# Performance work log

Hardware: AMD Instinct MI355X
Metric: run time of the kernel (lower is better)

## Reference

```python
import jax, jax.numpy as jnp
import numpy as np

N = 100000   # nodes
E = 50000    # hyperedges
K = 4        # nodes per hyperedge
D = 128      # out_dim (= in_dim here)
ED = 64      # edge_dim
H = 8        # num_heads


def _build_pairs(seed=0):
    # Sparse equivalent of the incidence-matrix nested loops:
    # for each edge e with member set S, emit ordered pairs (v, e, u) for v,u in S.
    rng = np.random.default_rng(seed)
    cover = rng.permutation(N).reshape(N // K, K)          # guarantees every node owns >=1 pair group
    rand = rng.integers(0, N, size=(E - N // K, K))
    edge_nodes = np.concatenate([cover, rand], axis=0)      # [E, K]
    owners = np.repeat(edge_nodes, K, axis=1).ravel()       # v, repeated K times per edge slot
    pair_u = np.tile(edge_nodes, (1, K)).ravel()            # u, tiled
    pair_e = np.repeat(np.arange(E), K * K)
    return owners.astype(np.int32), pair_e.astype(np.int32), pair_u.astype(np.int32)


def setup_inputs() -> dict:
    key = jax.random.key(0)
    ks = jax.random.split(key, 12)
    owners, pair_e, pair_u = _build_pairs()
    s = 0.05
    return {
        "x": jax.random.normal(ks[0], (N, D), jnp.float32),
        "edge_attr": jax.random.normal(ks[1], (E, ED), jnp.float32),
        "w_lin": jax.random.normal(ks[2], (D, D), jnp.float32) * s,   # self.lin (no bias)
        "w_e": jax.random.normal(ks[3], (ED, D), jnp.float32) * s,    # self.edge_lin (no bias)
        "w_q": jax.random.normal(ks[4], (D, D), jnp.float32) * s,
        "b_q": jax.random.normal(ks[5], (D,), jnp.float32) * s,
        "w_k": jax.random.normal(ks[6], (D, D), jnp.float32) * s,
        "b_k": jax.random.normal(ks[7], (D,), jnp.float32) * s,
        "w_v": jax.random.normal(ks[8], (D, D), jnp.float32) * s,
        "b_v": jax.random.normal(ks[9], (D,), jnp.float32) * s,
        "w_o": jax.random.normal(ks[10], (D, D), jnp.float32) * s,
        "b_o": jax.random.normal(ks[11], (D,), jnp.float32) * s,
        "owners": jnp.asarray(owners),
        "pair_e": jnp.asarray(pair_e),
        "pair_u": jnp.asarray(pair_u),
    }


def reference(x, edge_attr, w_lin, w_e, w_q, b_q, w_k, b_k, w_v, b_v, w_o, b_o, owners, pair_e, pair_u):
    n = x.shape[0]
    d = w_lin.shape[1]
    dh = d // H
    Wh = x @ w_lin                                  # [N, D]
    We = edge_attr @ w_e                            # [E, D]
    # Multi-head single-query attention per node over its (e,u) pair set.
    q = ((Wh @ w_q + b_q) / jnp.sqrt(jnp.asarray(dh, Wh.dtype))).reshape(n, H, dh)
    Wh_u = Wh[pair_u]                               # [P, D] value source (= Wh[u])
    k = ((Wh_u + We[pair_e]) @ w_k + b_k).reshape(-1, H, dh)   # key source = Wh[u] + We[e]
    v = (Wh_u @ w_v + b_v).reshape(-1, H, dh)
    scores = jnp.einsum('phd,phd->ph', q[owners], k)            # [P, H]
    # segmented (ragged) softmax over each node's pair set
    m = jax.ops.segment_max(scores, owners, num_segments=n)
    ex = jnp.exp(scores - m[owners])
    denom = jax.ops.segment_sum(ex, owners, num_segments=n)     # [N, H]
    alpha = ex / denom[owners]                                  # [P, H]
    ctx = jax.ops.segment_sum(alpha[..., None] * v, owners, num_segments=n).reshape(n, d)
    out = ctx @ w_o + b_o
    return jax.nn.relu(out)
```

## Files before the change

kernel.cpp:

```cpp
#include <hip/hip_runtime.h>

#define NN 100000
#define EE 50000
#define GG (EE*4)
#define NB 391

typedef __attribute__((ext_vector_type(8))) short bf16x8;
typedef __attribute__((ext_vector_type(4))) float f32x4;

__device__ __forceinline__ unsigned short f2bf(float f) {
  union { float f; unsigned int u; } c; c.f = f;
  unsigned int u = c.u;
  u = (u + 0x7fffu + ((u >> 16) & 1u)) >> 16;
  return (unsigned short)u;
}
__device__ __forceinline__ float bf2f(unsigned int lo16) {
  union { unsigned int u; float f; } c; c.u = lo16 << 16;
  return c.f;
}

struct __align__(8) us4 { unsigned short x, y, z, w; };

__global__ void k_prep(const float* __restrict__ w_lin, const float* __restrict__ w_e,
                       const float* __restrict__ w_q, const float* __restrict__ b_q,
                       const float* __restrict__ w_k, const float* __restrict__ b_k,
                       const float* __restrict__ w_v, const float* __restrict__ b_v,
                       const float* __restrict__ w_o, const float* __restrict__ b_o,
                       unsigned short* __restrict__ WT, unsigned short* __restrict__ WeT,
                       unsigned short* __restrict__ WoT, float* __restrict__ bias384,
                       float* __restrict__ bkB, float* __restrict__ boB) {
  int t = blockIdx.x * 256 + threadIdx.x;
  if (t < 49152) {
    int n = t >> 7, k = t & 127;
    const float* wsel; int nn; float scale = 1.0f;
    if (n < 128)      { wsel = w_q; nn = n;       scale = 0.25f; }
    else if (n < 256) { wsel = w_k; nn = n - 128; }
    else              { wsel = w_v; nn = n - 256; }
    float s = 0.f;
    for (int d = 0; d < 128; ++d) s += w_lin[k*128 + d] * wsel[d*128 + nn];
    WT[n*128 + k] = f2bf(s * scale);
  } else if (t < 57344) {
    int i = t - 49152, n = i >> 6, k = i & 63;
    float s = 0.f;
    for (int d = 0; d < 128; ++d) s += w_e[k*128 + d] * w_k[d*128 + n];
    WeT[n*64 + k] = f2bf(s);
  } else if (t < 73728) {
    int i = t - 57344, n = i >> 7, k = i & 127;
    WoT[n*128 + k] = f2bf(w_o[k*128 + n]);
  } else if (t < 74112) {
    int i = t - 73728;
    bias384[i] = (i < 128) ? b_q[i] * 0.25f : ((i < 256) ? 0.f : b_v[i - 256]);
  } else if (t < 74240) {
    bkB[t - 74112] = b_k[t - 74112];
  } else if (t < 74368) {
    boB[t - 74240] = b_o[t - 74240];
  }
}

__global__ __launch_bounds__(256) void k_qkv(const float* __restrict__ x,
                                             const unsigned short* __restrict__ WT,
                                             const float* __restrict__ bias,
                                             unsigned short* __restrict__ qkv) {
  __shared__ unsigned short As[64 * 136];
  int tid = threadIdx.x;
  int row0 = blockIdx.x * 64;
  #pragma unroll
  for (int it = 0; it < 8; ++it) {
    int i4 = tid + it * 256;
    int r = i4 >> 5, c4 = i4 & 31;
    float4 vv = make_float4(0.f, 0.f, 0.f, 0.f);
    int gr = row0 + r;
    if (gr < NN) vv = *(const float4*)(x + (size_t)gr * 128 + c4 * 4);
    us4 s4 = { f2bf(vv.x), f2bf(vv.y), f2bf(vv.z), f2bf(vv.w) };
    int chunk = c4 >> 1;
    int soff = r * 128 + ((chunk ^ (r & 7)) << 3) + ((c4 & 1) << 2);
    *(us4*)(&As[soff]) = s4;
  }
  __syncthreads();
  int w = tid >> 6, lane = tid & 63, lr = lane & 15, lk = lane >> 4;
  bf16x8 afr[4][4];
  #pragma unroll
  for (int rt = 0; rt < 4; ++rt) {
    int R = rt * 16 + lr;
    #pragma unroll
    for (int kk = 0; kk < 4; ++kk) {
      int chunk = (kk * 4 + lk) ^ (R & 7);
      afr[rt][kk] = *(const bf16x8*)(&As[R * 128 + chunk * 8]);
    }
  }
  #pragma unroll
  for (int p = 0; p < 3; ++p) {
    f32x4 acc[2][4] = {};
    #pragma unroll
    for (int h = 0; h < 2; ++h) {
      int gcol = p * 128 + h * 64 + w * 16 + lr;
      const unsigned short* bp = WT + (size_t)gcol * 128 + lk * 8;
      bf16x8 b0 = *(const bf16x8*)(bp);
      bf16x8 b1 = *(const bf16x8*)(bp + 32);
      bf16x8 b2 = *(const bf16x8*)(bp + 64);
      bf16x8 b3 = *(const bf16x8*)(bp + 96);
      #pragma unroll
      for (int rt = 0; rt < 4; ++rt) {
        acc[h][rt] = __builtin_amdgcn_mfma_f32_16x16x32_bf16(afr[rt][0], b0, acc[h][rt], 0, 0, 0);
        acc[h][rt] = __builtin_amdgcn_mfma_f32_16x16x32_bf16(afr[rt][1], b1, acc[h][rt], 0, 0, 0);
        acc[h][rt] = __builtin_amdgcn_mfma_f32_16x16x32_bf16(afr[rt][2], b2, acc[h][rt], 0, 0, 0);
        acc[h][rt] = __builtin_amdgcn_mfma_f32_16x16x32_bf16(afr[rt][3], b3, acc[h][rt], 0, 0, 0);
      }
    }
    __syncthreads();
    #pragma unroll
    for (int h = 0; h < 2; ++h) {
      int colp = h * 64 + w * 16 + lr;
      float b = bias[p * 128 + colp];
      #pragma unroll
      for (int rt = 0; rt < 4; ++rt) {
        #pragma unroll
        for (int j = 0; j < 4; ++j) {
          As[(rt * 16 + lk * 4 + j) * 136 + colp] = f2bf(acc[h][rt][j] + b);
        }
      }
    }
    __syncthreads();
    int piece = tid & 15, rbase = tid >> 4;
    #pragma unroll
    for (int it = 0; it < 4; ++it) {
      int r = rbase + it * 16;
      int grow = row0 + r;
      if (grow < NN) {
        float4 vv = *(const float4*)(&As[r * 136 + piece * 8]);
        *(float4*)(qkv + (size_t)grow * 384 + p * 128 + piece * 8) = vv;
      }
    }
  }
}

__global__ __launch_bounds__(256) void k_ke(const float* __restrict__ ea,
                                            const unsigned short* __restrict__ WeT,
                                            const float* __restrict__ bk,
                                            unsigned short* __restrict__ ke) {
  __shared__ unsigned short As[64][72];
  __shared__ unsigned short Bs[64][72];
  int tid = threadIdx.x;
  int row0 = blockIdx.x * 64;
  int col0 = blockIdx.y * 64;
  #pragma unroll
  for (int it = 0; it < 4; ++it) {
    int i4 = tid + it * 256;
    int r = i4 >> 4, c4 = i4 & 15;
    float4 vv = make_float4(0.f, 0.f, 0.f, 0.f);
    int gr = row0 + r;
    if (gr < EE) vv = *(const float4*)(ea + (size_t)gr * 64 + c4 * 4);
    us4 s4 = { f2bf(vv.x), f2bf(vv.y), f2bf(vv.z), f2bf(vv.w) };
    *(us4*)(&As[r][c4 * 4]) = s4;
  }
  #pragma unroll
  for (int it = 0; it < 4; ++it) {
    int i4 = tid + it * 256;
    int r = i4 >> 4, c4 = i4 & 15;
    us4 s4 = *(const us4*)(WeT + (size_t)(col0 + r) * 64 + c4 * 4);
    *(us4*)(&Bs[r][c4 * 4]) = s4;
  }
  __syncthreads();
  int w = tid >> 6, lane = tid & 63, lr = lane & 15, lk = lane >> 4;
  f32x4 acc[4] = {};
  #pragma unroll
  for (int kk = 0; kk < 2; ++kk) {
    int kof = kk * 32 + lk * 8;
    bf16x8 af = *(const bf16x8*)(&As[w * 16 + lr][kof]);
    #pragma unroll
    for (int nt = 0; nt < 4; ++nt) {
      bf16x8 bfrag = *(const bf16x8*)(&Bs[nt * 16 + lr][kof]);
      acc[nt] = __builtin_amdgcn_mfma_f32_16x16x32_bf16(af, bfrag, acc[nt], 0, 0, 0);
    }
  }
  #pragma unroll
  for (int nt = 0; nt < 4; ++nt) {
    int gcol = col0 + nt * 16 + lr;
    float b = bk[gcol];
    #pragma unroll
    for (int j = 0; j < 4; ++j) {
      int grow = row0 + w * 16 + lk * 4 + j;
      if (grow < EE) ke[(size_t)grow * 128 + gcol] = f2bf(acc[nt][j] + b);
    }
  }
}

__global__ void k_count(const int* __restrict__ owners, int* __restrict__ counts) {
  int g = blockIdx.x * 256 + threadIdx.x;
  if (g < GG) atomicAdd(counts + owners[(size_t)g * 4], 1);
}

__global__ __launch_bounds__(256) void k_scan1(const int* __restrict__ counts,
                                               int* __restrict__ lofs,
                                               int* __restrict__ bsums) {
  __shared__ int tmp[256];
  int tid = threadIdx.x;
  int i = blockIdx.x * 256 + tid;
  int v = (i < NN) ? counts[i] : 0;
  tmp[tid] = v;
  __syncthreads();
  int val = v;
  #pragma unroll
  for (int off = 1; off < 256; off <<= 1) {
    int t = (tid >= off) ? tmp[tid - off] : 0;
    __syncthreads();
    val += t;
    tmp[tid] = val;
    __syncthreads();
  }
  if (i < NN) lofs[i] = val - v;
  if (tid == 255) bsums[blockIdx.x] = val;
}

__global__ __launch_bounds__(512) void k_scan2(int* __restrict__ bsums) {
  __shared__ int tmp[512];
  int tid = threadIdx.x;
  int v = (tid < NB) ? bsums[tid] : 0;
  tmp[tid] = v;
  __syncthreads();
  int val = v;
  #pragma unroll
  for (int off = 1; off < 512; off <<= 1) {
    int t = (tid >= off) ? tmp[tid - off] : 0;
    __syncthreads();
    val += t;
    tmp[tid] = val;
    __syncthreads();
  }
  if (tid < NB) bsums[tid] = val - v;
}

__global__ void k_scan3(const int* __restrict__ lofs, const int* __restrict__ bsums,
                        int* __restrict__ starts, int* __restrict__ wcursor) {
  int i = blockIdx.x * 256 + threadIdx.x;
  if (i < NN) {
    int s = lofs[i] + bsums[i >> 8];
    starts[i] = s;
    wcursor[i] = s;
  }
  if (i == 0) starts[NN] = GG;
}

__global__ void k_scatter(const int* __restrict__ owners, int* __restrict__ wcursor,
                          int* __restrict__ pos) {
  int g = blockIdx.x * 256 + threadIdx.x;
  if (g < GG) {
    int v = owners[(size_t)g * 4];
    pos[g] = atomicAdd(wcursor + v, 1);
  }
}

__global__ __launch_bounds__(256) void k_edge(const unsigned short* __restrict__ qkv,
                                              const unsigned short* __restrict__ ke,
                                              const int* __restrict__ pair_u,
                                              const int* __restrict__ pos,
                                              unsigned short* __restrict__ pctx,
                                              float* __restrict__ pden) {
  int e = blockIdx.x * 4 + (threadIdx.x >> 6);
  if (e >= EE) return;
  int lane = threadIdx.x & 63;
  int m[4], ps[4];
  #pragma unroll
  for (int j = 0; j < 4; ++j) {
    m[j]  = __builtin_amdgcn_readfirstlane(pair_u[(size_t)e * 16 + j]);
    ps[j] = __builtin_amdgcn_readfirstlane(pos[(size_t)e * 4 + j]);
  }
  unsigned int kew = *(const unsigned int*)(ke + (size_t)e * 128 + 2 * lane);
  float e0 = bf2f(kew & 0xffffu), e1 = bf2f(kew >> 16);
  float qa[4][2], ka[4][2], va[4][2];
  #pragma unroll
  for (int j = 0; j < 4; ++j) {
    const unsigned short* r = qkv + (size_t)m[j] * 384 + 2 * lane;
    unsigned int qw = *(const unsigned int*)r;
    unsigned int kw = *(const unsigned int*)(r + 128);
    unsigned int vw = *(const unsigned int*)(r + 256);
    qa[j][0] = bf2f(qw & 0xffffu);      qa[j][1] = bf2f(qw >> 16);
    ka[j][0] = bf2f(kw & 0xffffu) + e0; ka[j][1] = bf2f(kw >> 16) + e1;
    va[j][0] = bf2f(vw & 0xffffu);      va[j][1] = bf2f(vw >> 16);
  }
  #pragma unroll
  for (int i = 0; i < 4; ++i) {
    float c0 = 0.f, c1 = 0.f, ds = 0.f;
    #pragma unroll
    for (int j = 0; j < 4; ++j) {
      float sc = qa[i][0] * ka[j][0] + qa[i][1] * ka[j][1];
      sc += __shfl_xor(sc, 1);
      sc += __shfl_xor(sc, 2);
      sc += __shfl_xor(sc, 4);
      float ex = __expf(sc);
      c0 += ex * va[j][0];
      c1 += ex * va[j][1];
      ds += ex;
    }
    unsigned int packed = (unsigned int)f2bf(c0) | ((unsigned int)f2bf(c1) << 16);
    *(unsigned int*)(pctx + (size_t)ps[i] * 128 + 2 * lane) = packed;
    if ((lane & 7) == 0) pden[(size_t)ps[i] * 8 + (lane >> 3)] = ds;
  }
}

__global__ __launch_bounds__(256) void k_out(const unsigned short* __restrict__ pctx,
                                             const float* __restrict__ pden,
                                             const int* __restrict__ starts,
                                             const unsigned short* __restrict__ WoT,
                                             const float* __restrict__ bo,
                                             float* __restrict__ out) {
  __shared__ unsigned short As[64][136];
  __shared__ unsigned short Bs[128][136];
  int tid = threadIdx.x;
  int row0 = blockIdx.x * 64;
  #pragma unroll
  for (int it = 0; it < 8; ++it) {
    int i4 = tid + it * 256;
    int r = i4 >> 5, c4 = i4 & 31;
    int gr = row0 + r;
    float a0 = 0.f, a1 = 0.f, a2 = 0.f, a3 = 0.f, ds = 0.f;
    if (gr < NN) {
      int s0 = starts[gr], s1 = starts[gr + 1];
      for (int sl = s0; sl < s1; ++sl) {
        us4 wv = *(const us4*)(pctx + (size_t)sl * 128 + c4 * 4);
        a0 += bf2f(wv.x); a1 += bf2f(wv.y); a2 += bf2f(wv.z); a3 += bf2f(wv.w);
        ds += pden[(size_t)sl * 8 + (c4 >> 2)];
      }
    }
    float inv = ds > 0.f ? 1.0f / ds : 0.f;
    us4 s4 = { f2bf(a0 * inv), f2bf(a1 * inv), f2bf(a2 * inv), f2bf(a3 * inv) };
    *(us4*)(&As[r][c4 * 4]) = s4;
  }
  #pragma unroll
  for (int it = 0; it < 16; ++it) {
    int i4 = tid + it * 256;
    int r = i4 >> 5, c4 = i4 & 31;
    *(us4*)(&Bs[r][c4 * 4]) = *(const us4*)(WoT + (size_t)r * 128 + c4 * 4);
  }
  __syncthreads();
  int w = tid >> 6, lane = tid & 63, lr = lane & 15, lk = lane >> 4;
  f32x4 acc[8] = {};
  #pragma unroll
  for (int kk = 0; kk < 4; ++kk) {
    int kof = kk * 32 + lk * 8;
    bf16x8 af = *(const bf16x8*)(&As[w * 16 + lr][kof]);
    #pragma unroll
    for (int nt = 0; nt < 8; ++nt) {
      bf16x8 bfrag = *(const bf16x8*)(&Bs[nt * 16 + lr][kof]);
      acc[nt] = __builtin_amdgcn_mfma_f32_16x16x32_bf16(af, bfrag, acc[nt], 0, 0, 0);
    }
  }
  #pragma unroll
  for (int nt = 0; nt < 8; ++nt) {
    int gcol = nt * 16 + lr;
    float b = bo[gcol];
    #pragma unroll
    for (int j = 0; j < 4; ++j) {
      int grow = row0 + w * 16 + lk * 4 + j;
      if (grow < NN) {
        float vvv = acc[nt][j] + b;
        out[(size_t)grow * 128 + gcol] = vvv > 0.f ? vvv : 0.f;
      }
    }
  }
}

extern "C" void kernel_launch(void* const* d_in, const int* in_sizes, int n_in,
                              void* d_out, int out_size, void* d_ws, size_t ws_size,
                              hipStream_t stream) {
  const float* x      = (const float*)d_in[0];
  const float* ea     = (const float*)d_in[1];
  const float* w_lin  = (const float*)d_in[2];
  const float* w_e    = (const float*)d_in[3];
  const float* w_q    = (const float*)d_in[4];
  const float* b_q    = (const float*)d_in[5];
  const float* w_k    = (const float*)d_in[6];
  const float* b_k    = (const float*)d_in[7];
  const float* w_v    = (const float*)d_in[8];
  const float* b_v    = (const float*)d_in[9];
  const float* w_o    = (const float*)d_in[10];
  const float* b_o    = (const float*)d_in[11];
  const int* owners   = (const int*)d_in[12];
  const int* pair_u   = (const int*)d_in[14];
  float* out = (float*)d_out;

  char* base = (char*)d_ws;
  size_t o = 0;
  auto alloc = [&](size_t b) {
    void* p = base + o;
    o = (o + b + 255) & ~(size_t)255;
    return p;
  };
  unsigned short* WT      = (unsigned short*)alloc((size_t)384 * 128 * 2);
  unsigned short* WeT     = (unsigned short*)alloc((size_t)128 * 64 * 2);
  unsigned short* WoT     = (unsigned short*)alloc((size_t)128 * 128 * 2);
  float* bias384          = (float*)alloc(384 * 4);
  float* bkB              = (float*)alloc(128 * 4);
  float* boB              = (float*)alloc(128 * 4);
  unsigned short* qkv     = (unsigned short*)alloc((size_t)NN * 384 * 2);
  unsigned short* keb     = (unsigned short*)alloc((size_t)EE * 128 * 2);
  int* counts             = (int*)alloc((size_t)NN * 4);
  int* starts             = (int*)alloc((size_t)(NN + 1) * 4);
  int* wcursor            = (int*)alloc((size_t)NN * 4);
  int* pos                = (int*)alloc((size_t)GG * 4);
  int* lofs               = (int*)alloc((size_t)NN * 4);
  int* bsums              = (int*)alloc((size_t)NB * 4);
  unsigned short* pctx    = (unsigned short*)alloc((size_t)GG * 128 * 2);
  float* pden             = (float*)alloc((size_t)GG * 8 * 4);

  hipMemsetAsync(counts, 0, (size_t)NN * 4, stream);

  k_prep<<<291, 256, 0, stream>>>(w_lin, w_e, w_q, b_q, w_k, b_k, w_v, b_v, w_o, b_o,
                                  WT, WeT, WoT, bias384, bkB, boB);
  k_qkv<<<1563, 256, 0, stream>>>(x, WT, bias384, qkv);
  k_ke<<<dim3(782, 2), 256, 0, stream>>>(ea, WeT, bkB, keb);
  k_count<<<782, 256, 0, stream>>>(owners, counts);
  k_scan1<<<NB, 256, 0, stream>>>(counts, lofs, bsums);
  k_scan2<<<1, 512, 0, stream>>>(bsums);
  k_scan3<<<NB, 256, 0, stream>>>(lofs, bsums, starts, wcursor);
  k_scatter<<<782, 256, 0, stream>>>(owners, wcursor, pos);
  k_edge<<<12500, 256, 0, stream>>>(qkv, keb, pair_u, pos, pctx, pden);
  k_out<<<1563, 256, 0, stream>>>(pctx, pden, starts, WoT, boB, out);
}
```

Measured before the change: 180.7 us.

## Drop LDS staging in output GEMM and process two hyperedges per wave

k_out no longer stages aggregated context rows and the Wo matrix in shared memory behind a block barrier. Each wave now gathers and normalizes 16 node rows straight into MFMA B-fragments, reads Wo fragments directly from global memory, and computes a transposed 16x16 product whose result is written as float4 stores. k_edge now handles two hyperedges per wave, raising memory-level parallelism on the gathered qkv rows and halving the grid. The trade-offs are more register pressure in both kernels and repeated global (cache-served) reads of Wo per wave instead of one shared copy per block.

```diff
diff --git a/kernel.cpp b/kernel.cpp
--- a/kernel.cpp
+++ b/kernel.cpp
@@ -17,6 +17,13 @@
 __device__ __forceinline__ float bf2f(unsigned int lo16) {
   union { unsigned int u; float f; } c; c.u = lo16 << 16;
   return c.f;
+}
+__device__ __forceinline__ bf16x8 pack8(const float* f) {
+  union { bf16x8 v; unsigned int u[4]; } r;
+  #pragma unroll
+  for (int i = 0; i < 4; ++i)
+    r.u[i] = (unsigned int)f2bf(f[2*i]) | ((unsigned int)f2bf(f[2*i+1]) << 16);
+  return r.v;
 }
 
 struct __align__(8) us4 { unsigned short x, y, z, w; };
@@ -256,46 +263,56 @@
                                               const int* __restrict__ pos,
                                               unsigned short* __restrict__ pctx,
                                               float* __restrict__ pden) {
-  int e = blockIdx.x * 4 + (threadIdx.x >> 6);
-  if (e >= EE) return;
+  int e0 = (blockIdx.x * 4 + (threadIdx.x >> 6)) * 2;
+  if (e0 >= EE) return;
   int lane = threadIdx.x & 63;
-  int m[4], ps[4];
-  #pragma unroll
-  for (int j = 0; j < 4; ++j) {
-    m[j]  = __builtin_amdgcn_readfirstlane(pair_u[(size_t)e * 16 + j]);
-    ps[j] = __builtin_amdgcn_readfirstlane(pos[(size_t)e * 4 + j]);
-  }
-  unsigned int kew = *(const unsigned int*)(ke + (size_t)e * 128 + 2 * lane);
-  float e0 = bf2f(kew & 0xffffu), e1 = bf2f(kew >> 16);
-  float qa[4][2], ka[4][2], va[4][2];
-  #pragma unroll
-  for (int j = 0; j < 4; ++j) {
-    const unsigned short* r = qkv + (size_t)m[j] * 384 + 2 * lane;
-    unsigned int qw = *(const unsigned int*)r;
-    unsigned int kw = *(const unsigned int*)(r + 128);
-    unsigned int vw = *(const unsigned int*)(r + 256);
-    qa[j][0] = bf2f(qw & 0xffffu);      qa[j][1] = bf2f(qw >> 16);
-    ka[j][0] = bf2f(kw & 0xffffu) + e0; ka[j][1] = bf2f(kw >> 16) + e1;
-    va[j][0] = bf2f(vw & 0xffffu);      va[j][1] = bf2f(vw >> 16);
-  }
-  #pragma unroll
-  for (int i = 0; i < 4; ++i) {
-    float c0 = 0.f, c1 = 0.f, ds = 0.f;
+  int m[2][4], ps[2][4];
+  #pragma unroll
+  for (int ee = 0; ee < 2; ++ee)
     #pragma unroll
     for (int j = 0; j < 4; ++j) {
-      float sc = qa[i][0] * ka[j][0] + qa[i][1] * ka[j][1];
-      sc += __shfl_xor(sc, 1);
-      sc += __shfl_xor(sc, 2);
-      sc += __shfl_xor(sc, 4);
-      float ex = __expf(sc);
-      c0 += ex * va[j][0];
-      c1 += ex * va[j][1];
-      ds += ex;
-    }
-    unsigned int packed = (unsigned int)f2bf(c0) | ((unsigned int)f2bf(c1) << 16);
-    *(unsigned int*)(pctx + (size_t)ps[i] * 128 + 2 * lane) = packed;
-    if ((lane & 7) == 0) pden[(size_t)ps[i] * 8 + (lane >> 3)] = ds;
-  }
+      m[ee][j]  = __builtin_amdgcn_readfirstlane(pair_u[(size_t)(e0 + ee) * 16 + j]);
+      ps[ee][j] = __builtin_amdgcn_readfirstlane(pos[(size_t)(e0 + ee) * 4 + j]);
+    }
+  float ev[2][2];
+  #pragma unroll
+  for (int ee = 0; ee < 2; ++ee) {
+    unsigned int kew = *(const unsigned int*)(ke + (size_t)(e0 + ee) * 128 + 2 * lane);
+    ev[ee][0] = bf2f(kew & 0xffffu); ev[ee][1] = bf2f(kew >> 16);
+  }
+  float qa[2][4][2], ka[2][4][2], va[2][4][2];
+  #pragma unroll
+  for (int ee = 0; ee < 2; ++ee)
+    #pragma unroll
+    for (int j = 0; j < 4; ++j) {
+      const unsigned short* r = qkv + (size_t)m[ee][j] * 384 + 2 * lane;
+      unsigned int qw = *(const unsigned int*)r;
+      unsigned int kw = *(const unsigned int*)(r + 128);
+      unsigned int vw = *(const unsigned int*)(r + 256);
+      qa[ee][j][0] = bf2f(qw & 0xffffu);             qa[ee][j][1] = bf2f(qw >> 16);
+      ka[ee][j][0] = bf2f(kw & 0xffffu) + ev[ee][0]; ka[ee][j][1] = bf2f(kw >> 16) + ev[ee][1];
+      va[ee][j][0] = bf2f(vw & 0xffffu);             va[ee][j][1] = bf2f(vw >> 16);
+    }
+  #pragma unroll
+  for (int ee = 0; ee < 2; ++ee)
+    #pragma unroll
+    for (int i = 0; i < 4; ++i) {
+      float c0 = 0.f, c1 = 0.f, ds = 0.f;
+      #pragma unroll
+      for (int j = 0; j < 4; ++j) {
+        float sc = qa[ee][i][0] * ka[ee][j][0] + qa[ee][i][1] * ka[ee][j][1];
+        sc += __shfl_xor(sc, 1);
+        sc += __shfl_xor(sc, 2);
+        sc += __shfl_xor(sc, 4);
+        float ex = __expf(sc);
+        c0 += ex * va[ee][j][0];
+        c1 += ex * va[ee][j][1];
+        ds += ex;
+      }
+      unsigned int packed = (unsigned int)f2bf(c0) | ((unsigned int)f2bf(c1) << 16);
+      *(unsigned int*)(pctx + (size_t)ps[ee][i] * 128 + 2 * lane) = packed;
+      if ((lane & 7) == 0) pden[(size_t)ps[ee][i] * 8 + (lane >> 3)] = ds;
+    }
 }
 
 __global__ __launch_bounds__(256) void k_out(const unsigned short* __restrict__ pctx,
@@ -304,59 +321,58 @@
                                              const unsigned short* __restrict__ WoT,
                                              const float* __restrict__ bo,
                                              float* __restrict__ out) {
-  __shared__ unsigned short As[64][136];
-  __shared__ unsigned short Bs[128][136];
-  int tid = threadIdx.x;
-  int row0 = blockIdx.x * 64;
-  #pragma unroll
-  for (int it = 0; it < 8; ++it) {
-    int i4 = tid + it * 256;
-    int r = i4 >> 5, c4 = i4 & 31;
-    int gr = row0 + r;
-    float a0 = 0.f, a1 = 0.f, a2 = 0.f, a3 = 0.f, ds = 0.f;
-    if (gr < NN) {
-      int s0 = starts[gr], s1 = starts[gr + 1];
-      for (int sl = s0; sl < s1; ++sl) {
-        us4 wv = *(const us4*)(pctx + (size_t)sl * 128 + c4 * 4);
-        a0 += bf2f(wv.x); a1 += bf2f(wv.y); a2 += bf2f(wv.z); a3 += bf2f(wv.w);
-        ds += pden[(size_t)sl * 8 + (c4 >> 2)];
-      }
-    }
-    float inv = ds > 0.f ? 1.0f / ds : 0.f;
-    us4 s4 = { f2bf(a0 * inv), f2bf(a1 * inv), f2bf(a2 * inv), f2bf(a3 * inv) };
-    *(us4*)(&As[r][c4 * 4]) = s4;
-  }
-  #pragma unroll
-  for (int it = 0; it < 16; ++it) {
-    int i4 = tid + it * 256;
-    int r = i4 >> 5, c4 = i4 & 31;
-    *(us4*)(&Bs[r][c4 * 4]) = *(const us4*)(WoT + (size_t)r * 128 + c4 * 4);
-  }
-  __syncthreads();
-  int w = tid >> 6, lane = tid & 63, lr = lane & 15, lk = lane >> 4;
-  f32x4 acc[8] = {};
+  int wid = blockIdx.x * 4 + (threadIdx.x >> 6);
+  if (wid >= NN / 16) return;
+  int lane = threadIdx.x & 63, lr = lane & 15, lk = lane >> 4;
+  int row = wid * 16 + lr;
+  float a[4][8];
+  float ds[4] = { 0.f, 0.f, 0.f, 0.f };
+  #pragma unroll
+  for (int kk = 0; kk < 4; ++kk)
+    #pragma unroll
+    for (int i = 0; i < 8; ++i) a[kk][i] = 0.f;
+  int s0 = starts[row], s1 = starts[row + 1];
+  for (int sl = s0; sl < s1; ++sl) {
+    const unsigned short* pr = pctx + (size_t)sl * 128 + lk * 8;
+    const float* dp = pden + (size_t)sl * 8 + (lk >> 1);
+    #pragma unroll
+    for (int kk = 0; kk < 4; ++kk) {
+      uint4 v = *(const uint4*)(pr + kk * 32);
+      a[kk][0] += bf2f(v.x & 0xffffu); a[kk][1] += bf2f(v.x >> 16);
+      a[kk][2] += bf2f(v.y & 0xffffu); a[kk][3] += bf2f(v.y >> 16);
+      a[kk][4] += bf2f(v.z & 0xffffu); a[kk][5] += bf2f(v.z >> 16);
+      a[kk][6] += bf2f(v.w & 0xffffu); a[kk][7] += bf2f(v.w >> 16);
+      ds[kk] += dp[kk * 2];
+    }
+  }
+  bf16x8 abf[4];
   #pragma unroll
   for (int kk = 0; kk < 4; ++kk) {
-    int kof = kk * 32 + lk * 8;
-    bf16x8 af = *(const bf16x8*)(&As[w * 16 + lr][kof]);
-    #pragma unroll
-    for (int nt = 0; nt < 8; ++nt) {
-      bf16x8 bfrag = *(const bf16x8*)(&Bs[nt * 16 + lr][kof]);
-      acc[nt] = __builtin_amdgcn_mfma_f32_16x16x32_bf16(af, bfrag, acc[nt], 0, 0, 0);
-    }
-  }
-  #pragma unroll
-  for (int nt = 0; nt < 8; ++nt) {
-    int gcol = nt * 16 + lr;
-    float b = bo[gcol];
-    #pragma unroll
-    for (int j = 0; j < 4; ++j) {
-      int grow = row0 + w * 16 + lk * 4 + j;
-      if (grow < NN) {
-        float vvv = acc[nt][j] + b;
-        out[(size_t)grow * 128 + gcol] = vvv > 0.f ? vvv : 0.f;
-      }
-    }
+    float inv = ds[kk] > 0.f ? 1.0f / ds[kk] : 0.f;
+    float f[8];
+    #pragma unroll
+    for (int i = 0; i < 8; ++i) f[i] = a[kk][i] * inv;
+    abf[kk] = pack8(f);
+  }
+  #pragma unroll
+  for (int ct = 0; ct < 8; ++ct) {
+    const unsigned short* wp = WoT + (size_t)(ct * 16 + lr) * 128 + lk * 8;
+    bf16x8 w0 = *(const bf16x8*)(wp);
+    bf16x8 w1 = *(const bf16x8*)(wp + 32);
+    bf16x8 w2 = *(const bf16x8*)(wp + 64);
+    bf16x8 w3 = *(const bf16x8*)(wp + 96);
+    f32x4 acc = {};
+    acc = __builtin_amdgcn_mfma_f32_16x16x32_bf16(w0, abf[0], acc, 0, 0, 0);
+    acc = __builtin_amdgcn_mfma_f32_16x16x32_bf16(w1, abf[1], acc, 0, 0, 0);
+    acc = __builtin_amdgcn_mfma_f32_16x16x32_bf16(w2, abf[2], acc, 0, 0, 0);
+    acc = __builtin_amdgcn_mfma_f32_16x16x32_bf16(w3, abf[3], acc, 0, 0, 0);
+    float4 bb = *(const float4*)(bo + ct * 16 + lk * 4);
+    float4 o;
+    o.x = fmaxf(acc[0] + bb.x, 0.f);
+    o.y = fmaxf(acc[1] + bb.y, 0.f);
+    o.z = fmaxf(acc[2] + bb.z, 0.f);
+    o.w = fmaxf(acc[3] + bb.w, 0.f);
+    *(float4*)(out + (size_t)row * 128 + ct * 16 + lk * 4) = o;
   }
 }
 
@@ -414,6 +430,6 @@
   k_scan2<<<1, 512, 0, stream>>>(bsums);
   k_scan3<<<NB, 256, 0, stream>>>(lofs, bsums, starts, wcursor);
   k_scatter<<<782, 256, 0, stream>>>(owners, wcursor, pos);
-  k_edge<<<12500, 256, 0, stream>>>(qkv, keb, pair_u, pos, pctx, pden);
+  k_edge<<<6250, 256, 0, stream>>>(qkv, keb, pair_u, pos, pctx, pden);
   k_out<<<1563, 256, 0, stream>>>(pctx, pden, starts, WoT, boB, out);
 }
```

Result: no change. 178.8 us (-1.0%).
